# Optimization experiments

Hardware: AMD Instinct MI355X
Metric: run time of the kernel (lower is better)

The kernel has to match this reference:

```python
import jax, jax.numpy as jnp
import numpy as np

LN_EPS = 1e-5


def _ssm_scan(x_ssm, A, Bm, C, reverse):
    # x_ssm: [B, L, d_inner]; A, Bm, C: [d_inner, d_state]
    Bb, L, di = x_ssm.shape
    ds = Bm.shape[1]

    def step(h, x_t):
        # h: [B, d_inner, d_state], x_t: [B, d_inner]
        h = jnp.clip(h * A[None] + x_t[:, :, None] * Bm[None], -10.0, 10.0)
        y = jnp.einsum('bid,id->bi', h, C)
        return h, y

    h0 = jnp.zeros((Bb, di, ds), x_ssm.dtype)
    _, ys = jax.lax.scan(step, h0, jnp.swapaxes(x_ssm, 0, 1), reverse=reverse)
    return jnp.swapaxes(ys, 0, 1)  # [B, L, d_inner], time-ordered


def setup_inputs() -> dict:
    key = jax.random.key(0)
    ks = jax.random.split(key, 6)
    B, L, D = 4, 2048, 1024
    d_state, expand = 16, 2
    d_inner = D * expand
    x = jax.random.normal(ks[0], (B, L, D), jnp.float32)
    # xavier-ish scaled params
    in_proj_w = jax.random.normal(ks[1], (d_inner * 2, D), jnp.float32) * np.float32(1.0 / np.sqrt(D))
    A_log = jax.random.normal(ks[2], (d_inner, d_state), jnp.float32)
    B_mat = jax.random.normal(ks[3], (d_inner, d_state), jnp.float32) * np.float32(1.0 / np.sqrt(d_state))
    C_mat = jnp.full((d_inner, d_state), 0.01, jnp.float32)
    out_proj_w = jax.random.normal(ks[4], (D, d_inner), jnp.float32) * np.float32(1.0 / np.sqrt(d_inner))
    ln_w = jnp.ones((D,), jnp.float32)
    ln_b = jnp.zeros((D,), jnp.float32)
    return {"x": x, "in_proj_w": in_proj_w, "A_log": A_log, "B_mat": B_mat,
            "C_mat": C_mat, "out_proj_w": out_proj_w, "ln_w": ln_w, "ln_b": ln_b}


def reference(x, in_proj_w, A_log, B_mat, C_mat, out_proj_w, ln_w, ln_b):
    # LayerNorm
    mu = jnp.mean(x, axis=-1, keepdims=True)
    var = jnp.mean((x - mu) ** 2, axis=-1, keepdims=True)
    xn = (x - mu) * jax.lax.rsqrt(var + LN_EPS) * ln_w + ln_b
    # in_proj (no bias), split into ssm stream and gate
    x_proj = jnp.einsum('bld,ed->ble', xn, in_proj_w)  # [B, L, 2*d_inner]
    x_ssm, gate = jnp.split(x_proj, 2, axis=-1)
    # A = -clamp(exp(A_log), -10, -0.01)  (saturates to 0.01, kept faithfully)
    A = -jnp.clip(jnp.exp(A_log), -10.0, -0.01)
    out_f = _ssm_scan(x_ssm, A, B_mat, C_mat, reverse=False)
    out_b = _ssm_scan(x_ssm, A, B_mat, C_mat, reverse=True)
    out = (out_f + out_b) * 0.5 * jax.nn.silu(gate)
    return jnp.einsum('bli,di->bld', out, out_proj_w)
```

## Files before the change

### kernel.cpp

```cpp
#include <hip/hip_runtime.h>

typedef __attribute__((ext_vector_type(8))) _Float16 f16x8;
typedef __attribute__((ext_vector_type(4))) float f32x4;

#define GLOBAL_AS __attribute__((address_space(1)))
#define LDS_AS __attribute__((address_space(3)))

static constexpr int Bb = 4, LL = 2048, DD = 1024, DI = 2048, DS = 16;
static constexpr int MROWS = Bb * LL;
static constexpr int N1 = 2 * DI;
static constexpr int K1 = DD;
static constexpr int N2 = DD;
static constexpr int K2 = DI;

__device__ __forceinline__ unsigned short f2h(float f) {
  _Float16 h = (_Float16)f;
  union { _Float16 h; unsigned short u; } c; c.h = h;
  return c.u;
}
__device__ __forceinline__ float h2f(unsigned short u) {
  union { unsigned short u; _Float16 h; } c; c.u = u;
  return (float)c.h;
}

__global__ __launch_bounds__(256) void ln_half_kernel(
    const float* __restrict__ x, const float* __restrict__ lnw,
    const float* __restrict__ lnb, unsigned short* __restrict__ A1) {
  const int r = blockIdx.x;
  const int tid = threadIdx.x;
  const float4 v = reinterpret_cast<const float4*>(x + (size_t)r * DD)[tid];
  float s = v.x + v.y + v.z + v.w;
#pragma unroll
  for (int off = 32; off >= 1; off >>= 1) s += __shfl_xor(s, off, 64);
  __shared__ float red[8];
  const int wid = tid >> 6;
  if ((tid & 63) == 0) red[wid] = s;
  __syncthreads();
  const float mu = (red[0] + red[1] + red[2] + red[3]) * (1.0f / DD);
  const float dx = v.x - mu, dy = v.y - mu, dz = v.z - mu, dw = v.w - mu;
  float ss = dx * dx + dy * dy + dz * dz + dw * dw;
#pragma unroll
  for (int off = 32; off >= 1; off >>= 1) ss += __shfl_xor(ss, off, 64);
  if ((tid & 63) == 0) red[4 + wid] = ss;
  __syncthreads();
  const float var = (red[4] + red[5] + red[6] + red[7]) * (1.0f / DD);
  const float rs = rsqrtf(var + 1e-5f);
  const float4 w4 = reinterpret_cast<const float4*>(lnw)[tid];
  const float4 b4 = reinterpret_cast<const float4*>(lnb)[tid];
  ushort4 h4;
  h4.x = f2h(dx * rs * w4.x + b4.x);
  h4.y = f2h(dy * rs * w4.y + b4.y);
  h4.z = f2h(dz * rs * w4.z + b4.z);
  h4.w = f2h(dw * rs * w4.w + b4.w);
  *reinterpret_cast<ushort4*>(&A1[(size_t)r * DD + tid * 4]) = h4;
}

__global__ __launch_bounds__(256) void f32_to_f16_kernel(
    const float* __restrict__ W, unsigned short* __restrict__ O) {
  const int gid = blockIdx.x * 256 + threadIdx.x;
  const float4 w = reinterpret_cast<const float4*>(W)[gid];
  ushort4 h4;
  h4.x = f2h(w.x); h4.y = f2h(w.y); h4.z = f2h(w.z); h4.w = f2h(w.w);
  reinterpret_cast<ushort4*>(O)[gid] = h4;
}

__global__ __launch_bounds__(512, 2) void gemm_bt_256(
    const unsigned short* __restrict__ A, const unsigned short* __restrict__ B,
    unsigned short* __restrict__ C, int M, int N, int K) {
  __shared__ unsigned short sm[2][2][256 * 64];
  const int tid = threadIdx.x;
  const int wid = tid >> 6;
  const int lane = tid & 63;
  const int wm = wid >> 2;
  const int wn = wid & 3;
  const int mt = M >> 8;
  const int cpx = gridDim.x >> 3;
  const int bid = blockIdx.x;
  const int sw = (bid & 7) * cpx + (bid >> 3);
  const int bm = sw % mt;
  const int bn = sw / mt;
  const size_t arow0 = (size_t)bm * 256;
  const size_t brow0 = (size_t)bn * 256;

  const unsigned short* gA[4];
  const unsigned short* gB[4];
#pragma unroll
  for (int j = 0; j < 4; ++j) {
    const int idx = j * 512 + tid;
    const int prow = idx >> 3;
    const int scol = ((idx & 7) ^ (prow & 7)) << 3;
    gA[j] = A + (arow0 + prow) * (size_t)K + scol;
    gB[j] = B + (brow0 + prow) * (size_t)K + scol;
  }
  auto stageA = [&](int buf) {
#pragma unroll
    for (int j = 0; j < 4; ++j) {
      __builtin_amdgcn_global_load_lds((const GLOBAL_AS void*)gA[j],
          (LDS_AS void*)&sm[buf][0][(j * 512 + (wid << 6)) * 8], 16, 0, 0);
      gA[j] += 64;
    }
  };
  auto stageB = [&](int buf) {
#pragma unroll
    for (int j = 0; j < 4; ++j) {
      __builtin_amdgcn_global_load_lds((const GLOBAL_AS void*)gB[j],
          (LDS_AS void*)&sm[buf][1][(j * 512 + (wid << 6)) * 8], 16, 0, 0);
      gB[j] += 64;
    }
  };

  const int q = lane >> 4;
  const int l7 = lane & 7;
  const int fr = lane & 15;
  int swz[2];
  swz[0] = (q << 3) ^ (l7 << 3);
  swz[1] = (32 + (q << 3)) ^ (l7 << 3);

  int arows[8], brows[4];
#pragma unroll
  for (int mf = 0; mf < 8; ++mf) arows[mf] = ((wm << 7) + mf * 16 + fr) * 64;
#pragma unroll
  for (int nf = 0; nf < 4; ++nf) brows[nf] = ((wn << 6) + nf * 16 + fr) * 64;

  f32x4 acc[8][4] = {};

  const int NTK = K >> 6;
  stageA(0);
  stageB(0);
  __syncthreads();

  for (int t = 0; t < NTK; ++t) {
    const int cur = t & 1, nxt = cur ^ 1;
    if (t + 1 < NTK) { stageA(nxt); stageB(nxt); }
    f16x8 af[8][2], bf[4][2];
#pragma unroll
    for (int mf = 0; mf < 8; ++mf)
#pragma unroll
      for (int ks = 0; ks < 2; ++ks)
        af[mf][ks] = *reinterpret_cast<const f16x8*>(&sm[cur][0][arows[mf] + swz[ks]]);
#pragma unroll
    for (int nf = 0; nf < 4; ++nf)
#pragma unroll
      for (int ks = 0; ks < 2; ++ks)
        bf[nf][ks] = *reinterpret_cast<const f16x8*>(&sm[cur][1][brows[nf] + swz[ks]]);
#pragma unroll
    for (int ks = 0; ks < 2; ++ks)
#pragma unroll
      for (int mf = 0; mf < 8; ++mf)
#pragma unroll
        for (int nf = 0; nf < 4; ++nf)
          acc[mf][nf] = __builtin_amdgcn_mfma_f32_16x16x32_f16(
              af[mf][ks], bf[nf][ks], acc[mf][nf], 0, 0, 0);
    __syncthreads();
  }

  const int fcol = lane & 15;
  const int frow4 = (lane >> 4) << 2;
#pragma unroll
  for (int mf = 0; mf < 8; ++mf)
#pragma unroll
    for (int nf = 0; nf < 4; ++nf) {
      const size_t row0 = arow0 + (wm << 7) + mf * 16 + frow4;
      const size_t col = brow0 + (wn << 6) + nf * 16 + fcol;
#pragma unroll
      for (int j = 0; j < 4; ++j)
        C[(row0 + j) * (size_t)N + col] = f2h(acc[mf][nf][j]);
    }
}

__global__ __launch_bounds__(512, 2) void gemm_bt_256n128(
    const unsigned short* __restrict__ A, const unsigned short* __restrict__ B,
    float* __restrict__ C, int M, int N, int K) {
  __shared__ unsigned short sm[2][24576];
  const int tid = threadIdx.x;
  const int wid = tid >> 6;
  const int lane = tid & 63;
  const int wm = wid >> 2;
  const int wn = wid & 3;
  const int mt = M >> 8;
  const int cpx = gridDim.x >> 3;
  const int bid = blockIdx.x;
  const int sw = (bid & 7) * cpx + (bid >> 3);
  const int bm = sw % mt;
  const int bn = sw / mt;
  const size_t arow0 = (size_t)bm * 256;
  const size_t brow0 = (size_t)bn * 128;

  const unsigned short* gA[4];
  const unsigned short* gB[2];
#pragma unroll
  for (int j = 0; j < 4; ++j) {
    const int idx = j * 512 + tid;
    const int prow = idx >> 3;
    const int scol = ((idx & 7) ^ (prow & 7)) << 3;
    gA[j] = A + (arow0 + prow) * (size_t)K + scol;
  }
#pragma unroll
  for (int j = 0; j < 2; ++j) {
    const int idx = j * 512 + tid;
    const int prow = idx >> 3;
    const int scol = ((idx & 7) ^ (prow & 7)) << 3;
    gB[j] = B + (brow0 + prow) * (size_t)K + scol;
  }
  auto stageA = [&](int buf) {
#pragma unroll
    for (int j = 0; j < 4; ++j) {
      __builtin_amdgcn_global_load_lds((const GLOBAL_AS void*)gA[j],
          (LDS_AS void*)&sm[buf][(j * 512 + (wid << 6)) * 8], 16, 0, 0);
      gA[j] += 64;
    }
  };
  auto stageB = [&](int buf) {
#pragma unroll
    for (int j = 0; j < 2; ++j) {
      __builtin_amdgcn_global_load_lds((const GLOBAL_AS void*)gB[j],
          (LDS_AS void*)&sm[buf][16384 + (j * 512 + (wid << 6)) * 8], 16, 0, 0);
      gB[j] += 64;
    }
  };

  const int q = lane >> 4;
  const int l7 = lane & 7;
  const int fr = lane & 15;
  int swz[2];
  swz[0] = (q << 3) ^ (l7 << 3);
  swz[1] = (32 + (q << 3)) ^ (l7 << 3);

  int arows[8], brows[2];
#pragma unroll
  for (int mf = 0; mf < 8; ++mf) arows[mf] = ((wm << 7) + mf * 16 + fr) * 64;
#pragma unroll
  for (int nf = 0; nf < 2; ++nf) brows[nf] = 16384 + ((wn << 5) + nf * 16 + fr) * 64;

  f32x4 acc[8][2] = {};

  const int NTK = K >> 6;
  stageA(0);
  stageB(0);
  __syncthreads();

  for (int t = 0; t < NTK; ++t) {
    const int cur = t & 1, nxt = cur ^ 1;
    if (t + 1 < NTK) { stageA(nxt); stageB(nxt); }
    f16x8 af[8][2], bf[2][2];
#pragma unroll
    for (int mf = 0; mf < 8; ++mf)
#pragma unroll
      for (int ks = 0; ks < 2; ++ks)
        af[mf][ks] = *reinterpret_cast<const f16x8*>(&sm[cur][arows[mf] + swz[ks]]);
#pragma unroll
    for (int nf = 0; nf < 2; ++nf)
#pragma unroll
      for (int ks = 0; ks < 2; ++ks)
        bf[nf][ks] = *reinterpret_cast<const f16x8*>(&sm[cur][brows[nf] + swz[ks]]);
#pragma unroll
    for (int ks = 0; ks < 2; ++ks)
#pragma unroll
      for (int mf = 0; mf < 8; ++mf)
#pragma unroll
        for (int nf = 0; nf < 2; ++nf)
          acc[mf][nf] = __builtin_amdgcn_mfma_f32_16x16x32_f16(
              af[mf][ks], bf[nf][ks], acc[mf][nf], 0, 0, 0);
    __syncthreads();
  }

  const int fcol = lane & 15;
  const int frow4 = (lane >> 4) << 2;
#pragma unroll
  for (int mf = 0; mf < 8; ++mf)
#pragma unroll
    for (int nf = 0; nf < 2; ++nf) {
      const size_t row0 = arow0 + (wm << 7) + mf * 16 + frow4;
      const size_t col = brow0 + (wn << 5) + nf * 16 + fcol;
#pragma unroll
      for (int j = 0; j < 4; ++j)
        C[(row0 + j) * (size_t)N + col] = acc[mf][nf][j];
    }
}

__global__ __launch_bounds__(256) void scan_kernel(
    const unsigned short* __restrict__ xp, const float* __restrict__ Bm,
    const float* __restrict__ Cm, unsigned short* __restrict__ oss) {
  constexpr int T = 32, KH = 8;
  const int blk = blockIdx.x;
  const int igrp = blk & 7;
  const int c = (blk >> 3) & 63;
  const int b = blk >> 9;
  const int tid = threadIdx.x;
  const int i = igrp * 256 + tid;
  float d = 0.f;
  {
    const float4* bp = reinterpret_cast<const float4*>(Bm + (size_t)i * DS);
    const float4* cp = reinterpret_cast<const float4*>(Cm + (size_t)i * DS);
#pragma unroll
    for (int qv = 0; qv < 4; ++qv) {
      const float4 bv = bp[qv], cv = cp[qv];
      d += bv.x * cv.x + bv.y * cv.y + bv.z * cv.z + bv.w * cv.w;
    }
  }
  const float dh = 0.5f * d;
  const int t0 = c * T;
  const size_t rowbase = (size_t)b * LL;
  float yf[T];
  float g = 0.f;
  {
    const int hstart = (t0 >= KH) ? t0 - KH : 0;
    for (int t = hstart; t < t0; ++t)
      g = fmaf(0.01f, g, h2f(xp[(rowbase + t) * (size_t)N1 + i]));
#pragma unroll
    for (int j = 0; j < T; ++j) {
      g = fmaf(0.01f, g, h2f(xp[(rowbase + t0 + j) * (size_t)N1 + i]));
      yf[j] = g;
    }
  }
  g = 0.f;
  {
    const int tend = (t0 + T - 1 + KH <= LL - 1) ? (t0 + T - 1 + KH) : (LL - 1);
    for (int t = tend; t >= t0 + T; --t)
      g = fmaf(0.01f, g, h2f(xp[(rowbase + t) * (size_t)N1 + i]));
#pragma unroll
    for (int j = T - 1; j >= 0; --j) {
      const size_t row = rowbase + t0 + j;
      g = fmaf(0.01f, g, h2f(xp[row * (size_t)N1 + i]));
      const float gt = h2f(xp[row * (size_t)N1 + DI + i]);
      const float sg = gt / (1.f + expf(-gt));
      const float o = (yf[j] + g) * dh * sg;
      oss[row * (size_t)DI + i] = f2h(o);
    }
  }
}

extern "C" void kernel_launch(void* const* d_in, const int* in_sizes, int n_in,
                              void* d_out, int out_size, void* d_ws, size_t ws_size,
                              hipStream_t stream) {
  (void)in_sizes; (void)n_in; (void)out_size; (void)ws_size;
  const float* x          = (const float*)d_in[0];
  const float* in_proj_w  = (const float*)d_in[1];
  const float* B_mat      = (const float*)d_in[3];
  const float* C_mat      = (const float*)d_in[4];
  const float* out_proj_w = (const float*)d_in[5];
  const float* ln_w       = (const float*)d_in[6];
  const float* ln_b       = (const float*)d_in[7];
  float* out = (float*)d_out;

  char* ws = (char*)d_ws;
  unsigned short* A1  = (unsigned short*)ws; ws += (size_t)MROWS * K1 * 2;
  unsigned short* B1  = (unsigned short*)ws; ws += (size_t)N1 * K1 * 2;
  unsigned short* B2  = (unsigned short*)ws; ws += (size_t)N2 * K2 * 2;
  unsigned short* OSS = (unsigned short*)ws; ws += (size_t)MROWS * DI * 2;
  unsigned short* XP  = (unsigned short*)ws; ws += (size_t)MROWS * N1 * 2;

  f32_to_f16_kernel<<<dim3((N1 * K1 / 4) / 256), dim3(256), 0, stream>>>(in_proj_w, B1);
  f32_to_f16_kernel<<<dim3((N2 * K2 / 4) / 256), dim3(256), 0, stream>>>(out_proj_w, B2);
  ln_half_kernel<<<dim3(MROWS), dim3(256), 0, stream>>>(x, ln_w, ln_b, A1);
  gemm_bt_256<<<dim3((MROWS / 256) * (N1 / 256)), dim3(512), 0, stream>>>(A1, B1, XP, MROWS, N1, K1);
  scan_kernel<<<dim3(2048), dim3(256), 0, stream>>>(XP, B_mat, C_mat, OSS);
  gemm_bt_256n128<<<dim3((MROWS / 256) * (N2 / 128)), dim3(512), 0, stream>>>(OSS, B2, out, MROWS, N2, K2);
}
```

Before: 181.9 us.

## Use 4-slot K=32 ring buffer with prefetch distance two in GEMM

Restructures the 256x256 GEMM mainloop from a double-buffered K=64 stage to a four-slot ring of K=32 stages with loads issued two iterations ahead. Completion is tracked with explicit vmcnt waits and a single barrier per iteration instead of syncthreads after compute, and the LDS swizzle is changed to match the narrower rows. The aim is to hide global-to-LDS latency better and remove one barrier per step. In exchange each iteration does half as much MFMA work between barriers, and correctness depends on the hand-written vmcnt counts and the slot-reuse distance.

After: 189.3 us. 1.04x slower.

```diff
diff --git a/kernel.cpp b/kernel.cpp
--- a/kernel.cpp
+++ b/kernel.cpp
@@ -67,7 +67,7 @@
 __global__ __launch_bounds__(512, 2) void gemm_bt_256(
     const unsigned short* __restrict__ A, const unsigned short* __restrict__ B,
     unsigned short* __restrict__ C, int M, int N, int K) {
-  __shared__ unsigned short sm[2][2][256 * 64];
+  __shared__ unsigned short sm[4][2][256 * 32];
   const int tid = threadIdx.x;
   const int wid = tid >> 6;
   const int lane = tid & 63;
@@ -82,76 +82,68 @@
   const size_t arow0 = (size_t)bm * 256;
   const size_t brow0 = (size_t)bn * 256;
 
-  const unsigned short* gA[4];
-  const unsigned short* gB[4];
-#pragma unroll
-  for (int j = 0; j < 4; ++j) {
+  const unsigned short* gA[2];
+  const unsigned short* gB[2];
+#pragma unroll
+  for (int j = 0; j < 2; ++j) {
     const int idx = j * 512 + tid;
-    const int prow = idx >> 3;
-    const int scol = ((idx & 7) ^ (prow & 7)) << 3;
+    const int prow = idx >> 2;
+    const int scol = ((idx & 3) ^ (prow & 3)) << 3;
     gA[j] = A + (arow0 + prow) * (size_t)K + scol;
     gB[j] = B + (brow0 + prow) * (size_t)K + scol;
   }
-  auto stageA = [&](int buf) {
-#pragma unroll
-    for (int j = 0; j < 4; ++j) {
+  auto stage = [&](int slot) {
+#pragma unroll
+    for (int j = 0; j < 2; ++j) {
       __builtin_amdgcn_global_load_lds((const GLOBAL_AS void*)gA[j],
-          (LDS_AS void*)&sm[buf][0][(j * 512 + (wid << 6)) * 8], 16, 0, 0);
-      gA[j] += 64;
+          (LDS_AS void*)&sm[slot][0][(j * 512 + tid) * 8], 16, 0, 0);
+      gA[j] += 32;
+    }
+#pragma unroll
+    for (int j = 0; j < 2; ++j) {
+      __builtin_amdgcn_global_load_lds((const GLOBAL_AS void*)gB[j],
+          (LDS_AS void*)&sm[slot][1][(j * 512 + tid) * 8], 16, 0, 0);
+      gB[j] += 32;
     }
   };
-  auto stageB = [&](int buf) {
-#pragma unroll
-    for (int j = 0; j < 4; ++j) {
-      __builtin_amdgcn_global_load_lds((const GLOBAL_AS void*)gB[j],
-          (LDS_AS void*)&sm[buf][1][(j * 512 + (wid << 6)) * 8], 16, 0, 0);
-      gB[j] += 64;
-    }
-  };
 
   const int q = lane >> 4;
-  const int l7 = lane & 7;
   const int fr = lane & 15;
-  int swz[2];
-  swz[0] = (q << 3) ^ (l7 << 3);
-  swz[1] = (32 + (q << 3)) ^ (l7 << 3);
+  const int swzk = ((q ^ (fr & 3)) << 3);
 
   int arows[8], brows[4];
 #pragma unroll
-  for (int mf = 0; mf < 8; ++mf) arows[mf] = ((wm << 7) + mf * 16 + fr) * 64;
-#pragma unroll
-  for (int nf = 0; nf < 4; ++nf) brows[nf] = ((wn << 6) + nf * 16 + fr) * 64;
+  for (int mf = 0; mf < 8; ++mf) arows[mf] = ((wm << 7) + mf * 16 + fr) * 32;
+#pragma unroll
+  for (int nf = 0; nf < 4; ++nf) brows[nf] = ((wn << 6) + nf * 16 + fr) * 32;
 
   f32x4 acc[8][4] = {};
 
-  const int NTK = K >> 6;
-  stageA(0);
-  stageB(0);
-  __syncthreads();
+  const int NTK = K >> 5;
+  stage(0);
+  stage(1);
 
   for (int t = 0; t < NTK; ++t) {
-    const int cur = t & 1, nxt = cur ^ 1;
-    if (t + 1 < NTK) { stageA(nxt); stageB(nxt); }
-    f16x8 af[8][2], bf[4][2];
+    const int slot = t & 3;
+    if (t + 2 < NTK) stage((t + 2) & 3);
+    if (t + 2 < NTK)      asm volatile("s_waitcnt vmcnt(8)" ::: "memory");
+    else if (t + 1 < NTK) asm volatile("s_waitcnt vmcnt(4)" ::: "memory");
+    else                  asm volatile("s_waitcnt vmcnt(0)" ::: "memory");
+    __builtin_amdgcn_s_barrier();
+    __builtin_amdgcn_sched_barrier(0);
+    f16x8 af[8], bf[4];
 #pragma unroll
     for (int mf = 0; mf < 8; ++mf)
-#pragma unroll
-      for (int ks = 0; ks < 2; ++ks)
-        af[mf][ks] = *reinterpret_cast<const f16x8*>(&sm[cur][0][arows[mf] + swz[ks]]);
+      af[mf] = *reinterpret_cast<const f16x8*>(&sm[slot][0][arows[mf] + swzk]);
 #pragma unroll
     for (int nf = 0; nf < 4; ++nf)
-#pragma unroll
-      for (int ks = 0; ks < 2; ++ks)
-        bf[nf][ks] = *reinterpret_cast<const f16x8*>(&sm[cur][1][brows[nf] + swz[ks]]);
-#pragma unroll
-    for (int ks = 0; ks < 2; ++ks)
-#pragma unroll
-      for (int mf = 0; mf < 8; ++mf)
-#pragma unroll
-        for (int nf = 0; nf < 4; ++nf)
-          acc[mf][nf] = __builtin_amdgcn_mfma_f32_16x16x32_f16(
-              af[mf][ks], bf[nf][ks], acc[mf][nf], 0, 0, 0);
-    __syncthreads();
+      bf[nf] = *reinterpret_cast<const f16x8*>(&sm[slot][1][brows[nf] + swzk]);
+#pragma unroll
+    for (int mf = 0; mf < 8; ++mf)
+#pragma unroll
+      for (int nf = 0; nf < 4; ++nf)
+        acc[mf][nf] = __builtin_amdgcn_mfma_f32_16x16x32_f16(
+            af[mf], bf[nf], acc[mf][nf], 0, 0, 0);
   }
 
   const int fcol = lane & 15;
```
